# Kernel optimization log

Measured on AMD Instinct MI355X. Metric: run time of the kernel, lower is better.

Reference implementation:

```python
import jax, jax.numpy as jnp
import numpy as np


def _sage_layer(x_src, x_dst, src, dst, n_dst, W_neigh, W_self, b):
    # mean aggregation of src features onto dst nodes (zero for isolated dst)
    msgs = x_src[src]                                            # [E, d_in]
    summed = jax.ops.segment_sum(msgs, dst, num_segments=n_dst)  # [n_dst, d_in]
    deg = jax.ops.segment_sum(jnp.ones_like(dst, dtype=x_src.dtype), dst,
                              num_segments=n_dst)                # [n_dst]
    mean = summed / jnp.maximum(deg, 1)[:, None]
    # DGL SAGEConv('mean'): fc_self(h_dst) + fc_neigh(h_mean) + bias
    return x_dst @ W_self + mean @ W_neigh + b


def setup_inputs() -> dict:
    key = jax.random.key(0)
    ks = jax.random.split(key, 12)
    N_SRC, D_IN, HID, OUT = 100000, 128, 256, 64
    SIZE1, SIZE2 = 25000, 5000
    E1, E2 = 800000, 160000

    def glorot(k, shape):
        lim = np.sqrt(6.0 / (shape[0] + shape[1])).astype(np.float32)
        return jax.random.uniform(k, shape, jnp.float32, -lim, lim)

    return {
        "x": jax.random.normal(ks[0], (N_SRC, D_IN), jnp.float32),
        "W_self1": glorot(ks[1], (D_IN, HID)),
        "W_neigh1": glorot(ks[2], (D_IN, HID)),
        "b1": jnp.zeros((HID,), jnp.float32),
        "W_self2": glorot(ks[3], (HID, OUT)),
        "W_neigh2": glorot(ks[4], (HID, OUT)),
        "b2": jnp.zeros((OUT,), jnp.float32),
        "edge_src1": jax.random.randint(ks[5], (E1,), 0, N_SRC, jnp.int32),
        "edge_dst1": jax.random.randint(ks[6], (E1,), 0, SIZE1, jnp.int32),
        "edge_src2": jax.random.randint(ks[7], (E2,), 0, SIZE1, jnp.int32),
        "edge_dst2": jax.random.randint(ks[8], (E2,), 0, SIZE2, jnp.int32),
        "size1": SIZE1,
        "size2": SIZE2,
    }


def reference(x, W_self1, W_neigh1, b1, W_self2, W_neigh2, b2,
              edge_src1, edge_dst1, edge_src2, edge_dst2, size1, size2):
    # Layer 1: src = all nodes, dst = first size1 nodes
    h = _sage_layer(x, x[:size1], edge_src1, edge_dst1, size1,
                    W_neigh1, W_self1, b1)
    h = jax.nn.relu(h)  # dropout is identity in eval mode
    # Layer 2: src = layer-1 outputs (size1 nodes), dst = first size2 nodes
    h = _sage_layer(h, h[:size2], edge_src2, edge_dst2, size2,
                    W_neigh2, W_self2, b2)
    return jax.nn.log_softmax(h, axis=-1)
```

## Files before the change

kernel.cpp:

```cpp
#include <hip/hip_runtime.h>


constexpr int D_IN  = 128;
constexpr int HID   = 256;
constexpr int OUT_D = 64;
constexpr int SIZE1 = 25000;
constexpr int SIZE2 = 5000;
constexpr int SEGC  = 16;
constexpr int OVFS  = 48;
constexpr int ROW   = 8 * SEGC + OVFS;
constexpr int ECH   = 2048;

using bf16x8 = __attribute__((ext_vector_type(8))) short;
using f32x4  = __attribute__((ext_vector_type(4))) float;

__device__ inline unsigned short f32_to_bf16_rne(float f) {
    unsigned u = __builtin_bit_cast(unsigned, f);
    u = (u + 0x7fffu + ((u >> 16) & 1u)) >> 16;
    return (unsigned short)u;
}
__device__ inline float bf16_lo(unsigned u) {
    return __builtin_bit_cast(float, u << 16);
}
__device__ inline float bf16_hi(unsigned u) {
    return __builtin_bit_cast(float, u & 0xffff0000u);
}
__device__ inline unsigned pack_bf16(float lo, float hi) {
    return (unsigned)f32_to_bf16_rne(lo) | ((unsigned)f32_to_bf16_rne(hi) << 16);
}
__device__ inline void add8(float* a, uint4 v) {
    a[0] += bf16_lo(v.x); a[1] += bf16_hi(v.x);
    a[2] += bf16_lo(v.y); a[3] += bf16_hi(v.y);
    a[4] += bf16_lo(v.z); a[5] += bf16_hi(v.z);
    a[6] += bf16_lo(v.w); a[7] += bf16_hi(v.w);
}

__device__ inline void fill_body(const int* __restrict__ es,
                                 const int* __restrict__ ed, int E, int base0,
                                 int* __restrict__ cnt, int* __restrict__ ovf,
                                 int* __restrict__ csr) {
    int xcc;
    asm volatile("s_getreg_b32 %0, hwreg(HW_REG_XCC_ID)" : "=s"(xcc));
    xcc &= 7;
#pragma unroll
    for (int j = 0; j < ECH / 256; ++j) {
        int e = base0 + j * 256;
        if (e < E) {
            int d = ed[e];
            int pos = atomicAdd(&cnt[d * 8 + xcc], 1);
            if (pos < SEGC) {
                csr[(long)d * ROW + xcc * SEGC + pos] = es[e];
            } else {
                int po = atomicAdd(&ovf[d], 1);
                if (po < OVFS) csr[(long)d * ROW + 8 * SEGC + po] = es[e];
            }
        }
    }
}

__global__ void megafuse(const int* __restrict__ es1, const int* __restrict__ ed1,
                         int E1, int* __restrict__ cnt1, int* __restrict__ ovf1,
                         int* __restrict__ csr1,
                         const float* __restrict__ x, unsigned* __restrict__ xb,
                         long n4,
                         const float* __restrict__ Ws1, const float* __restrict__ Wn1,
                         const float* __restrict__ Ws2, const float* __restrict__ Wn2,
                         unsigned short* __restrict__ Wt1,
                         unsigned short* __restrict__ Wt2,
                         int f1, int f2) {
    const int b = blockIdx.x;
    const int tid = threadIdx.x;
    if (b < f1) {
        fill_body(es1, ed1, E1, b * ECH + tid, cnt1, ovf1, csr1);
    } else if (b < f2) {
        long i0 = (long)(b - f1) * 512 + tid;
#pragma unroll
        for (int j = 0; j < 2; ++j) {
            long i = i0 + j * 256;
            if (i < n4) {
                float4 v = reinterpret_cast<const float4*>(x)[i];
                uint2 o;
                o.x = pack_bf16(v.x, v.y);
                o.y = pack_bf16(v.z, v.w);
                reinterpret_cast<uint2*>(xb)[i] = o;
            }
        }
    } else {
        int i = (b - f2) * 256 + tid;
        if (i < HID * (2 * D_IN)) {
            int n = i >> 8, k = i & 255;
            float v = (k < D_IN) ? Ws1[k * HID + n] : Wn1[(k - D_IN) * HID + n];
            Wt1[i] = f32_to_bf16_rne(v);
        } else {
            int j = i - HID * (2 * D_IN);
            if (j < OUT_D * (2 * HID)) {
                int n = j >> 9, k = j & 511;
                float v = (k < HID) ? Ws2[k * OUT_D + n] : Wn2[(k - HID) * OUT_D + n];
                Wt2[j] = f32_to_bf16_rne(v);
            }
        }
    }
}

template <int QPL, bool FUSE>
__global__ void agg_pull5(const uint4* __restrict__ X4,
                          const int* __restrict__ csr,
                          const int* __restrict__ cnt,
                          const int* __restrict__ ovf,
                          uint4* __restrict__ mean4, int ndst, int aggBlocks,
                          const int* __restrict__ esF, const int* __restrict__ edF,
                          int EF, int* __restrict__ cntF, int* __restrict__ ovfF,
                          int* __restrict__ csrF) {
    if (FUSE && (int)blockIdx.x >= aggBlocks) {
        fill_body(esF, edF, EF, ((int)blockIdx.x - aggBlocks) * ECH + threadIdx.x,
                  cntF, ovfF, csrF);
        return;
    }
    constexpr int R4 = QPL * 16;
    const int wid = threadIdx.x >> 6;
    const int lane = threadIdx.x & 63;
    const int d = blockIdx.x * 4 + wid;
    if (d >= ndst) return;

    int myc = 0;
    if (lane < 8) myc = min(cnt[d * 8 + lane], SEGC);
    else if (lane == 8) myc = min(ovf[d], OVFS);
    int cum[10];
    cum[0] = 0;
#pragma unroll
    for (int k = 0; k < 9; ++k) cum[k + 1] = cum[k] + __shfl(myc, k);
    const int n = cum[9];
    const long rowb = (long)d * ROW;

    int slot = lane;
#pragma unroll
    for (int t = 1; t < 9; ++t)
        if (lane >= cum[t]) slot = (t < 8 ? t * SEGC : 8 * SEGC) + (lane - cum[t]);
    int myidx = 0;
    if (lane < n) myidx = csr[rowb + slot];

    const int g = lane >> 4;
    const int c = lane & 15;
    const int nmain = min(n, 64);

    float acc[QPL][8];
#pragma unroll
    for (int q = 0; q < QPL; ++q)
#pragma unroll
        for (int j = 0; j < 8; ++j) acc[q][j] = 0.0f;

    const int nI8 = nmain >> 5;
    for (int i = 0; i < nI8; ++i) {
        const int e0 = i * 32 + g;
        int s[8];
#pragma unroll
        for (int t = 0; t < 8; ++t) s[t] = __shfl(myidx, e0 + 4 * t);
#pragma unroll
        for (int q = 0; q < QPL; ++q) {
            uint4 v[8];
#pragma unroll
            for (int t = 0; t < 8; ++t) v[t] = X4[(long)s[t] * R4 + q * 16 + c];
#pragma unroll
            for (int t = 0; t < 8; ++t) add8(acc[q], v[t]);
        }
    }
    if (nI8 * 32 < nmain) {
        const int e0 = nI8 * 32 + g;
        int s[8];
#pragma unroll
        for (int t = 0; t < 8; ++t) s[t] = __shfl(myidx, (e0 + 4 * t) & 63);
#pragma unroll
        for (int t = 0; t < 8; ++t) {
            if (e0 + 4 * t < nmain) {
#pragma unroll
                for (int q = 0; q < QPL; ++q) {
                    uint4 v = X4[(long)s[t] * R4 + q * 16 + c];
                    add8(acc[q], v);
                }
            }
        }
    }
    for (int j2 = 64 + g; j2 < n; j2 += 4) {
        int sl = j2;
#pragma unroll
        for (int t = 1; t < 9; ++t)
            if (j2 >= cum[t]) sl = (t < 8 ? t * SEGC : 8 * SEGC) + (j2 - cum[t]);
        long s0 = csr[rowb + sl];
#pragma unroll
        for (int q = 0; q < QPL; ++q) {
            uint4 v0 = X4[s0 * R4 + q * 16 + c];
            add8(acc[q], v0);
        }
    }
#pragma unroll
    for (int q = 0; q < QPL; ++q)
#pragma unroll
        for (int jj = 0; jj < 8; ++jj) {
            acc[q][jj] += __shfl_xor(acc[q][jj], 16);
            acc[q][jj] += __shfl_xor(acc[q][jj], 32);
        }
    if (g == 0) {
        const float inv = 1.0f / (float)max(n, 1);
#pragma unroll
        for (int q = 0; q < QPL; ++q) {
            uint4 o;
            o.x = pack_bf16(acc[q][0] * inv, acc[q][1] * inv);
            o.y = pack_bf16(acc[q][2] * inv, acc[q][3] * inv);
            o.z = pack_bf16(acc[q][4] * inv, acc[q][5] * inv);
            o.w = pack_bf16(acc[q][6] * inv, acc[q][7] * inv);
            mean4[(long)d * R4 + q * 16 + c] = o;
        }
    }
}

template <int KPH, bool RELU, bool OUT_BF16, bool LSM>
__global__ __launch_bounds__(256) void sage_gemm_mfma(
    const unsigned short* __restrict__ Aself,
    const unsigned short* __restrict__ Amean,
    const unsigned short* __restrict__ Wt,
    const float* __restrict__ bias,
    void* __restrict__ Cout, int M, int N) {
    constexpr int BM = 64, BN = 64;
    constexpr int ITERS = (BM * KPH) / (256 * 8);
    __shared__ unsigned short As[BM * KPH];
    __shared__ unsigned short Bs[BN * KPH];

    const int tid = threadIdx.x;
    const int wid = tid >> 6;
    const int lane = tid & 63;
    const int wm = wid >> 1, wn = wid & 1;
    const int rowBase = blockIdx.x * BM;
    const int colBase = blockIdx.y * BN;

    f32x4 acc[2][2];
#pragma unroll
    for (int a = 0; a < 2; ++a)
#pragma unroll
        for (int b = 0; b < 2; ++b)
#pragma unroll
            for (int j = 0; j < 4; ++j) acc[a][b][j] = 0.0f;

#pragma unroll
    for (int p = 0; p < 2; ++p) {
        const unsigned short* __restrict__ A = p ? Amean : Aself;
        __syncthreads();
#pragma unroll
        for (int it = 0; it < ITERS; ++it) {
            int flat = (it * 256 + tid) * 8;
            int r = flat / KPH, kc = flat % KPH;
            int gr = rowBase + r;
            if (gr >= M) gr = M - 1;
            uint4 v = *reinterpret_cast<const uint4*>(&A[(long)gr * KPH + kc]);
            int idx = (r * KPH + kc) ^ ((r & 7) << 3);
            *reinterpret_cast<uint4*>(&As[idx]) = v;
        }
#pragma unroll
        for (int it = 0; it < ITERS; ++it) {
            int flat = (it * 256 + tid) * 8;
            int r = flat / KPH, kc = flat % KPH;
            uint4 v = *reinterpret_cast<const uint4*>(
                &Wt[(long)(colBase + r) * (2 * KPH) + p * KPH + kc]);
            int idx = (r * KPH + kc) ^ ((r & 7) << 3);
            *reinterpret_cast<uint4*>(&Bs[idx]) = v;
        }
        __syncthreads();
#pragma unroll
        for (int kk = 0; kk < KPH / 32; ++kk) {
            bf16x8 a[2], b[2];
            const int kb = kk * 32 + 8 * (lane >> 4);
#pragma unroll
            for (int f = 0; f < 2; ++f) {
                int r = wm * 32 + f * 16 + (lane & 15);
                int ia = (r * KPH + kb) ^ ((r & 7) << 3);
                a[f] = *reinterpret_cast<const bf16x8*>(&As[ia]);
                int rn = wn * 32 + f * 16 + (lane & 15);
                int ib = (rn * KPH + kb) ^ ((rn & 7) << 3);
                b[f] = *reinterpret_cast<const bf16x8*>(&Bs[ib]);
            }
#pragma unroll
            for (int fm = 0; fm < 2; ++fm)
#pragma unroll
                for (int fn = 0; fn < 2; ++fn)
                    acc[fm][fn] = __builtin_amdgcn_mfma_f32_16x16x32_bf16(
                        a[fm], b[fn], acc[fm][fn], 0, 0, 0);
        }
    }

    if (LSM) {
        float* sm = reinterpret_cast<float*>(As);
        __syncthreads();
#pragma unroll
        for (int fm = 0; fm < 2; ++fm)
#pragma unroll
            for (int fn = 0; fn < 2; ++fn) {
                int c = wn * 32 + fn * 16 + (lane & 15);
                float bv = bias[colBase + c];
#pragma unroll
                for (int j = 0; j < 4; ++j) {
                    int r = wm * 32 + fm * 16 + 4 * (lane >> 4) + j;
                    sm[r * BN + c] = acc[fm][fn][j] + bv;
                }
            }
        __syncthreads();
        for (int rr = 0; rr < 16; ++rr) {
            int r = wid * 16 + rr;
            int gr = rowBase + r;
            if (gr >= M) continue;
            float v = sm[r * BN + lane];
            float m = v;
#pragma unroll
            for (int o = 32; o; o >>= 1) m = fmaxf(m, __shfl_xor(m, o));
            float ex = __expf(v - m);
            float s = ex;
#pragma unroll
            for (int o = 32; o; o >>= 1) s += __shfl_xor(s, o);
            ((float*)Cout)[(long)gr * N + lane] = v - m - __logf(s);
        }
    } else {
#pragma unroll
        for (int fm = 0; fm < 2; ++fm) {
#pragma unroll
            for (int fn = 0; fn < 2; ++fn) {
                int gc = colBase + wn * 32 + fn * 16 + (lane & 15);
                float bv = bias[gc];
#pragma unroll
                for (int j = 0; j < 4; ++j) {
                    int gr = rowBase + wm * 32 + fm * 16 + 4 * (lane >> 4) + j;
                    if (gr < M) {
                        float v = acc[fm][fn][j] + bv;
                        if (RELU) v = fmaxf(v, 0.0f);
                        if (OUT_BF16)
                            ((unsigned short*)Cout)[(long)gr * N + gc] =
                                f32_to_bf16_rne(v);
                        else
                            ((float*)Cout)[(long)gr * N + gc] = v;
                    }
                }
            }
        }
    }
}


extern "C" void kernel_launch(void* const* d_in, const int* in_sizes, int n_in,
                              void* d_out, int out_size, void* d_ws, size_t ws_size,
                              hipStream_t stream) {
    const float* x       = (const float*)d_in[0];
    const float* Wself1  = (const float*)d_in[1];
    const float* Wneigh1 = (const float*)d_in[2];
    const float* b1      = (const float*)d_in[3];
    const float* Wself2  = (const float*)d_in[4];
    const float* Wneigh2 = (const float*)d_in[5];
    const float* b2      = (const float*)d_in[6];
    const int* es1 = (const int*)d_in[7];
    const int* ed1 = (const int*)d_in[8];
    const int* es2 = (const int*)d_in[9];
    const int* ed2 = (const int*)d_in[10];
    const int E1 = in_sizes[7];
    const int E2 = in_sizes[9];
    const long NSRC = in_sizes[0] / D_IN;

    int* cnt1 = (int*)d_ws;
    int* ovf1 = cnt1 + (size_t)SIZE1 * 8;
    int* cnt2 = ovf1 + SIZE1;
    int* ovf2 = cnt2 + (size_t)SIZE2 * 8;
    int* csr2 = ovf2 + SIZE2;
    int* csr1 = csr2 + (size_t)SIZE2 * ROW;
    const size_t zero_ints = (size_t)SIZE1 * 9 + (size_t)SIZE2 * 9;
    const size_t int_elems = zero_ints + (size_t)SIZE2 * ROW + (size_t)SIZE1 * ROW;
    unsigned short* xb    = (unsigned short*)((int*)d_ws + int_elems);
    unsigned short* mean2 = xb;
    unsigned short* Wt1   = xb + NSRC * D_IN;
    unsigned short* Wt2   = Wt1 + (size_t)HID * (2 * D_IN);
    unsigned short* mean1 = Wt2 + (size_t)OUT_D * (2 * HID);
    unsigned short* h1    = (unsigned short*)csr1;

    hipMemsetAsync(d_ws, 0, zero_ints * sizeof(int), stream);

    const long n4 = NSRC * D_IN / 4;
    const int f1 = (E1 + ECH - 1) / ECH;
    const int f2 = f1 + (int)((n4 + 511) / 512);
    const int nb_cw = (HID * (2 * D_IN) + OUT_D * (2 * HID) + 255) / 256;
    megafuse<<<f2 + nb_cw, 256, 0, stream>>>(
        es1, ed1, E1, cnt1, ovf1, csr1,
        x, (unsigned*)xb, n4, Wself1, Wneigh1, Wself2, Wneigh2, Wt1, Wt2,
        f1, f2);

    {
        const int aggB = (SIZE1 + 3) / 4;
        const int fillB = (E2 + ECH - 1) / ECH;
        agg_pull5<1, true><<<aggB + fillB, 256, 0, stream>>>(
            (const uint4*)xb, csr1, cnt1, ovf1, (uint4*)mean1, SIZE1, aggB,
            es2, ed2, E2, cnt2, ovf2, csr2);
    }
    {
        dim3 grid((SIZE1 + 63) / 64, HID / 64);
        sage_gemm_mfma<D_IN, true, true, false><<<grid, 256, 0, stream>>>(
            xb, mean1, Wt1, b1, h1, SIZE1, HID);
    }

    agg_pull5<2, false><<<(SIZE2 + 3) / 4, 256, 0, stream>>>(
        (const uint4*)h1, csr2, cnt2, ovf2, (uint4*)mean2, SIZE2, 1 << 30,
        nullptr, nullptr, 0, nullptr, nullptr, nullptr);
    {
        dim3 grid((SIZE2 + 63) / 64, OUT_D / 64);
        sage_gemm_mfma<HID, false, false, true><<<grid, 256, 0, stream>>>(
            h1, mean2, Wt2, b2, d_out, SIZE2, OUT_D);
    }
}
```

Baseline: 152.2 us.

## Gather neighbor features in fp8 for both aggregation layers

Result: faster. 129.9 us (-14.7%).

```diff
diff --git a/kernel.cpp b/kernel.cpp
--- a/kernel.cpp
+++ b/kernel.cpp
@@ -13,26 +13,25 @@
 
 using bf16x8 = __attribute__((ext_vector_type(8))) short;
 using f32x4  = __attribute__((ext_vector_type(4))) float;
+using f32x2  = __attribute__((ext_vector_type(2))) float;
 
 __device__ inline unsigned short f32_to_bf16_rne(float f) {
     unsigned u = __builtin_bit_cast(unsigned, f);
     u = (u + 0x7fffu + ((u >> 16) & 1u)) >> 16;
     return (unsigned short)u;
 }
-__device__ inline float bf16_lo(unsigned u) {
-    return __builtin_bit_cast(float, u << 16);
-}
-__device__ inline float bf16_hi(unsigned u) {
-    return __builtin_bit_cast(float, u & 0xffff0000u);
-}
 __device__ inline unsigned pack_bf16(float lo, float hi) {
     return (unsigned)f32_to_bf16_rne(lo) | ((unsigned)f32_to_bf16_rne(hi) << 16);
 }
-__device__ inline void add8(float* a, uint4 v) {
-    a[0] += bf16_lo(v.x); a[1] += bf16_hi(v.x);
-    a[2] += bf16_lo(v.y); a[3] += bf16_hi(v.y);
-    a[4] += bf16_lo(v.z); a[5] += bf16_hi(v.z);
-    a[6] += bf16_lo(v.w); a[7] += bf16_hi(v.w);
+__device__ inline void add16(float* a, uint4 v) {
+    const unsigned u[4] = {v.x, v.y, v.z, v.w};
+#pragma unroll
+    for (int i = 0; i < 4; ++i) {
+        f32x2 f0 = __builtin_amdgcn_cvt_pk_f32_fp8(u[i], false);
+        f32x2 f1 = __builtin_amdgcn_cvt_pk_f32_fp8(u[i], true);
+        a[i * 4 + 0] += f0.x; a[i * 4 + 1] += f0.y;
+        a[i * 4 + 2] += f1.x; a[i * 4 + 3] += f1.y;
+    }
 }
 
 __device__ inline void fill_body(const int* __restrict__ es,
@@ -61,8 +60,8 @@
 __global__ void megafuse(const int* __restrict__ es1, const int* __restrict__ ed1,
                          int E1, int* __restrict__ cnt1, int* __restrict__ ovf1,
                          int* __restrict__ csr1,
-                         const float* __restrict__ x, unsigned* __restrict__ xb,
-                         long n4,
+                         const float* __restrict__ x, unsigned* __restrict__ xbu,
+                         unsigned* __restrict__ x8u, long n4,
                          const float* __restrict__ Ws1, const float* __restrict__ Wn1,
                          const float* __restrict__ Ws2, const float* __restrict__ Wn2,
                          unsigned short* __restrict__ Wt1,
@@ -79,10 +78,15 @@
             long i = i0 + j * 256;
             if (i < n4) {
                 float4 v = reinterpret_cast<const float4*>(x)[i];
-                uint2 o;
-                o.x = pack_bf16(v.x, v.y);
-                o.y = pack_bf16(v.z, v.w);
-                reinterpret_cast<uint2*>(xb)[i] = o;
+                int p = __builtin_amdgcn_cvt_pk_fp8_f32(v.x, v.y, 0, false);
+                p = __builtin_amdgcn_cvt_pk_fp8_f32(v.z, v.w, p, true);
+                x8u[i] = (unsigned)p;
+                if (i < (long)SIZE1 * (D_IN / 4)) {
+                    uint2 o;
+                    o.x = pack_bf16(v.x, v.y);
+                    o.y = pack_bf16(v.z, v.w);
+                    reinterpret_cast<uint2*>(xbu)[i] = o;
+                }
             }
         }
     } else {
@@ -102,12 +106,12 @@
     }
 }
 
-template <int QPL, bool FUSE>
-__global__ void agg_pull5(const uint4* __restrict__ X4,
+template <int GL, bool FUSE>
+__global__ void agg_pull6(const uint4* __restrict__ X4,
                           const int* __restrict__ csr,
                           const int* __restrict__ cnt,
                           const int* __restrict__ ovf,
-                          uint4* __restrict__ mean4, int ndst, int aggBlocks,
+                          uint4* __restrict__ meanOut, int ndst, int aggBlocks,
                           const int* __restrict__ esF, const int* __restrict__ edF,
                           int EF, int* __restrict__ cntF, int* __restrict__ ovfF,
                           int* __restrict__ csrF) {
@@ -116,7 +120,8 @@
                   cntF, ovfF, csrF);
         return;
     }
-    constexpr int R4 = QPL * 16;
+    constexpr int NG = 64 / GL;
+    constexpr int NR = (64 + NG * 8 - 1) / (NG * 8);
     const int wid = threadIdx.x >> 6;
     const int lane = threadIdx.x & 63;
     const int d = blockIdx.x * 4 + wid;
@@ -139,87 +144,73 @@
     int myidx = 0;
     if (lane < n) myidx = csr[rowb + slot];
 
-    const int g = lane >> 4;
-    const int c = lane & 15;
+    const int g = lane / GL;
+    const int c = lane % GL;
     const int nmain = min(n, 64);
 
-    float acc[QPL][8];
-#pragma unroll
-    for (int q = 0; q < QPL; ++q)
-#pragma unroll
-        for (int j = 0; j < 8; ++j) acc[q][j] = 0.0f;
-
-    const int nI8 = nmain >> 5;
-    for (int i = 0; i < nI8; ++i) {
-        const int e0 = i * 32 + g;
-        int s[8];
-#pragma unroll
-        for (int t = 0; t < 8; ++t) s[t] = __shfl(myidx, e0 + 4 * t);
-#pragma unroll
-        for (int q = 0; q < QPL; ++q) {
+    float acc[16];
+#pragma unroll
+    for (int j = 0; j < 16; ++j) acc[j] = 0.0f;
+
+#pragma unroll
+    for (int r = 0; r < NR; ++r) {
+        const int base = r * NG * 8;
+        if (base < nmain) {
+            int s[8];
+            bool act[8];
+#pragma unroll
+            for (int t = 0; t < 8; ++t) {
+                const int e = base + g + NG * t;
+                int ss = __shfl(myidx, e & 63);
+                act[t] = (e < nmain);
+                s[t] = act[t] ? ss : 0;
+            }
             uint4 v[8];
 #pragma unroll
-            for (int t = 0; t < 8; ++t) v[t] = X4[(long)s[t] * R4 + q * 16 + c];
-#pragma unroll
-            for (int t = 0; t < 8; ++t) add8(acc[q], v[t]);
-        }
-    }
-    if (nI8 * 32 < nmain) {
-        const int e0 = nI8 * 32 + g;
-        int s[8];
-#pragma unroll
-        for (int t = 0; t < 8; ++t) s[t] = __shfl(myidx, (e0 + 4 * t) & 63);
-#pragma unroll
-        for (int t = 0; t < 8; ++t) {
-            if (e0 + 4 * t < nmain) {
-#pragma unroll
-                for (int q = 0; q < QPL; ++q) {
-                    uint4 v = X4[(long)s[t] * R4 + q * 16 + c];
-                    add8(acc[q], v);
-                }
-            }
-        }
-    }
-    for (int j2 = 64 + g; j2 < n; j2 += 4) {
+            for (int t = 0; t < 8; ++t) v[t] = X4[(long)s[t] * GL + c];
+#pragma unroll
+            for (int t = 0; t < 8; ++t)
+                if (act[t]) add16(acc, v[t]);
+        }
+    }
+    for (int j2 = 64 + g; j2 < n; j2 += NG) {
         int sl = j2;
 #pragma unroll
         for (int t = 1; t < 9; ++t)
             if (j2 >= cum[t]) sl = (t < 8 ? t * SEGC : 8 * SEGC) + (j2 - cum[t]);
         long s0 = csr[rowb + sl];
-#pragma unroll
-        for (int q = 0; q < QPL; ++q) {
-            uint4 v0 = X4[s0 * R4 + q * 16 + c];
-            add8(acc[q], v0);
-        }
-    }
-#pragma unroll
-    for (int q = 0; q < QPL; ++q)
-#pragma unroll
-        for (int jj = 0; jj < 8; ++jj) {
-            acc[q][jj] += __shfl_xor(acc[q][jj], 16);
-            acc[q][jj] += __shfl_xor(acc[q][jj], 32);
-        }
+        uint4 v0 = X4[s0 * GL + c];
+        add16(acc, v0);
+    }
+#pragma unroll
+    for (int j = 0; j < 16; ++j) {
+        if (GL == 8) acc[j] += __shfl_xor(acc[j], 8);
+        acc[j] += __shfl_xor(acc[j], 16);
+        acc[j] += __shfl_xor(acc[j], 32);
+    }
     if (g == 0) {
         const float inv = 1.0f / (float)max(n, 1);
-#pragma unroll
-        for (int q = 0; q < QPL; ++q) {
-            uint4 o;
-            o.x = pack_bf16(acc[q][0] * inv, acc[q][1] * inv);
-            o.y = pack_bf16(acc[q][2] * inv, acc[q][3] * inv);
-            o.z = pack_bf16(acc[q][4] * inv, acc[q][5] * inv);
-            o.w = pack_bf16(acc[q][6] * inv, acc[q][7] * inv);
-            mean4[(long)d * R4 + q * 16 + c] = o;
-        }
-    }
-}
-
-template <int KPH, bool RELU, bool OUT_BF16, bool LSM>
+        uint4 o0, o1;
+        o0.x = pack_bf16(acc[0] * inv, acc[1] * inv);
+        o0.y = pack_bf16(acc[2] * inv, acc[3] * inv);
+        o0.z = pack_bf16(acc[4] * inv, acc[5] * inv);
+        o0.w = pack_bf16(acc[6] * inv, acc[7] * inv);
+        o1.x = pack_bf16(acc[8] * inv, acc[9] * inv);
+        o1.y = pack_bf16(acc[10] * inv, acc[11] * inv);
+        o1.z = pack_bf16(acc[12] * inv, acc[13] * inv);
+        o1.w = pack_bf16(acc[14] * inv, acc[15] * inv);
+        meanOut[(long)d * (GL * 2) + c * 2]     = o0;
+        meanOut[(long)d * (GL * 2) + c * 2 + 1] = o1;
+    }
+}
+
+template <int KPH, bool RELU, bool OUT_BF16, bool LSM, bool H8>
 __global__ __launch_bounds__(256) void sage_gemm_mfma(
     const unsigned short* __restrict__ Aself,
     const unsigned short* __restrict__ Amean,
     const unsigned short* __restrict__ Wt,
     const float* __restrict__ bias,
-    void* __restrict__ Cout, int M, int N) {
+    void* __restrict__ Cout, unsigned char* __restrict__ H8out, int M, int N) {
     constexpr int BM = 64, BN = 64;
     constexpr int ITERS = (BM * KPH) / (256 * 8);
     __shared__ unsigned short As[BM * KPH];
@@ -334,6 +325,10 @@
                                 f32_to_bf16_rne(v);
                         else
                             ((float*)Cout)[(long)gr * N + gc] = v;
+                        if (H8) {
+                            int b8 = __builtin_amdgcn_cvt_pk_fp8_f32(v, v, 0, false);
+                            H8out[(long)gr * N + gc] = (unsigned char)(b8 & 0xff);
+                        }
                     }
                 }
             }
@@ -368,12 +363,14 @@
     int* csr1 = csr2 + (size_t)SIZE2 * ROW;
     const size_t zero_ints = (size_t)SIZE1 * 9 + (size_t)SIZE2 * 9;
     const size_t int_elems = zero_ints + (size_t)SIZE2 * ROW + (size_t)SIZE1 * ROW;
-    unsigned short* xb    = (unsigned short*)((int*)d_ws + int_elems);
+    unsigned short* xb  = (unsigned short*)((int*)d_ws + int_elems);
     unsigned short* mean2 = xb;
-    unsigned short* Wt1   = xb + NSRC * D_IN;
-    unsigned short* Wt2   = Wt1 + (size_t)HID * (2 * D_IN);
+    unsigned char* x8   = (unsigned char*)(xb + (size_t)SIZE1 * D_IN);
+    unsigned short* Wt1 = (unsigned short*)(x8 + NSRC * D_IN);
+    unsigned short* Wt2 = Wt1 + (size_t)HID * (2 * D_IN);
     unsigned short* mean1 = Wt2 + (size_t)OUT_D * (2 * HID);
-    unsigned short* h1    = (unsigned short*)csr1;
+    unsigned char* h8   = (unsigned char*)(mean1 + (size_t)SIZE1 * D_IN);
+    unsigned short* h1  = (unsigned short*)csr1;
 
     hipMemsetAsync(d_ws, 0, zero_ints * sizeof(int), stream);
 
@@ -383,28 +380,28 @@
     const int nb_cw = (HID * (2 * D_IN) + OUT_D * (2 * HID) + 255) / 256;
     megafuse<<<f2 + nb_cw, 256, 0, stream>>>(
         es1, ed1, E1, cnt1, ovf1, csr1,
-        x, (unsigned*)xb, n4, Wself1, Wneigh1, Wself2, Wneigh2, Wt1, Wt2,
-        f1, f2);
+        x, (unsigned*)xb, (unsigned*)x8, n4,
+        Wself1, Wneigh1, Wself2, Wneigh2, Wt1, Wt2, f1, f2);
 
     {
         const int aggB = (SIZE1 + 3) / 4;
         const int fillB = (E2 + ECH - 1) / ECH;
-        agg_pull5<1, true><<<aggB + fillB, 256, 0, stream>>>(
-            (const uint4*)xb, csr1, cnt1, ovf1, (uint4*)mean1, SIZE1, aggB,
+        agg_pull6<8, true><<<aggB + fillB, 256, 0, stream>>>(
+            (const uint4*)x8, csr1, cnt1, ovf1, (uint4*)mean1, SIZE1, aggB,
             es2, ed2, E2, cnt2, ovf2, csr2);
     }
     {
         dim3 grid((SIZE1 + 63) / 64, HID / 64);
-        sage_gemm_mfma<D_IN, true, true, false><<<grid, 256, 0, stream>>>(
-            xb, mean1, Wt1, b1, h1, SIZE1, HID);
-    }
-
-    agg_pull5<2, false><<<(SIZE2 + 3) / 4, 256, 0, stream>>>(
-        (const uint4*)h1, csr2, cnt2, ovf2, (uint4*)mean2, SIZE2, 1 << 30,
+        sage_gemm_mfma<D_IN, true, true, false, true><<<grid, 256, 0, stream>>>(
+            xb, mean1, Wt1, b1, h1, h8, SIZE1, HID);
+    }
+
+    agg_pull6<16, false><<<(SIZE2 + 3) / 4, 256, 0, stream>>>(
+        (const uint4*)h8, csr2, cnt2, ovf2, (uint4*)mean2, SIZE2, 1 << 30,
         nullptr, nullptr, 0, nullptr, nullptr, nullptr);
     {
         dim3 grid((SIZE2 + 63) / 64, OUT_D / 64);
-        sage_gemm_mfma<HID, false, false, true><<<grid, 256, 0, stream>>>(
-            h1, mean2, Wt2, b2, d_out, SIZE2, OUT_D);
-    }
-}
+        sage_gemm_mfma<HID, false, false, true, false><<<grid, 256, 0, stream>>>(
+            h1, mean2, Wt2, b2, d_out, nullptr, SIZE2, OUT_D);
+    }
+}
```
